# Performance work log

Measured on AMD Instinct MI355X. Metric: run time of the kernel, lower is better.

Reference implementation:

```python
import jax, jax.numpy as jnp
import numpy as np

N = 100000
E = 3200000
CH_IN = 128
HID = 128
CH_OUT = 3


def setup_inputs() -> dict:
    key = jax.random.key(0)
    ks = jax.random.split(key, 16)
    def lin(kw, fan_in, fan_out):
        bound = 1.0 / np.sqrt(fan_in)
        kw1, kw2 = jax.random.split(kw)
        W = jax.random.uniform(kw1, (fan_in, fan_out), jnp.float32, -bound, bound)
        b = jax.random.uniform(kw2, (fan_out,), jnp.float32, -bound, bound)
        return W, b
    x = jax.random.normal(ks[0], (N, CH_IN), jnp.float32)
    edge_index = jax.random.randint(ks[1], (2, E), 0, N, jnp.int64)
    W1, b1 = lin(ks[2], CH_IN, HID)
    W2, b2 = lin(ks[3], HID, HID)
    lw1, lb1 = lin(ks[4], HID, HID)
    lw2, lb2 = lin(ks[5], HID, HID)
    lw3, lb3 = lin(ks[6], HID, HID)
    lw4, lb4 = lin(ks[7], HID, CH_OUT)
    return {"x": x, "edge_index": edge_index,
            "W1": W1, "b1": b1, "W2": W2, "b2": b2,
            "lw1": lw1, "lb1": lb1, "lw2": lw2, "lb2": lb2,
            "lw3": lw3, "lb3": lb3, "lw4": lw4, "lb4": lb4}


def gcn_conv(x, W, b, src, dst, n_nodes):
    xw = x @ W  # [N, H]
    ew = jnp.ones(src.shape[0], x.dtype)
    deg = jax.ops.segment_sum(ew, dst, num_segments=n_nodes) + 2.0  # +2 from improved self-loop
    dinv = jnp.where(deg > 0, jax.lax.rsqrt(deg), 0.0)
    norm = dinv[src] * dinv[dst]  # [E]
    agg = jax.ops.segment_sum(xw[src] * norm[:, None], dst, num_segments=n_nodes)
    # self-loop contribution: weight 2 * dinv[i]^2 * xw[i]
    agg = agg + xw * (2.0 * dinv * dinv)[:, None]
    return agg + b


def reference(x, edge_index, W1, b1, W2, b2, lw1, lb1, lw2, lb2, lw3, lb3, lw4, lb4):
    src, dst = edge_index[0], edge_index[1]
    n = x.shape[0]
    h = jnp.tanh(gcn_conv(x, W1, b1, src, dst, n))
    h = jnp.tanh(gcn_conv(h, W2, b2, src, dst, n))
    # dropout in eval mode = identity
    h = jnp.tanh(h @ lw1 + lb1)
    h = jnp.tanh(h @ lw2 + lb2)
    h = jnp.tanh(h @ lw3 + lb3)
    return h @ lw4 + lb4
```

## Files before the change

### kernel.cpp

```cpp
#include <hip/hip_runtime.h>

typedef __attribute__((ext_vector_type(8))) short short8;
typedef __attribute__((ext_vector_type(4))) float floatx4;
typedef __attribute__((ext_vector_type(4))) unsigned int uintx4;
typedef unsigned int uint32;

__device__ inline float b2f(unsigned short u) {
    union { uint32 i; float f; } x; x.i = ((uint32)u) << 16; return x.f;
}
__device__ inline float bl(uint32 v) {
    union { uint32 i; float f; } x; x.i = v << 16; return x.f;
}
__device__ inline float bh(uint32 v) {
    union { uint32 i; float f; } x; x.i = v & 0xffff0000u; return x.f;
}
__device__ inline unsigned short f2b(float f) {
    union { float f; uint32 u; } x; x.f = f;
    uint32 r = x.u + 0x7fffu + ((x.u >> 16) & 1u);
    return (unsigned short)(r >> 16);
}
__device__ inline float fast_tanh(float x) {
    float ax = __builtin_fabsf(x);
    float t = __builtin_amdgcn_exp2f(-2.8853900817779268f * ax);
    float r = (1.0f - t) * __builtin_amdgcn_rcpf(1.0f + t);
    return __builtin_copysignf(r, x);
}


#define CHUNK 8192
#define MAXBK 512
#define CAP   8704

__global__ __launch_bounds__(512, 2) void scatterb_k(const int* __restrict__ eidx,
                                                     uint32* __restrict__ bkt_cur,
                                                     uint32* __restrict__ packed, int E) {
    __shared__ uint32 hist[MAXBK];
    __shared__ uint32 ssum[MAXBK];
    __shared__ uint32 hsc[MAXBK];
    __shared__ uint32 gbase[MAXBK];
    __shared__ uint32 lcur[MAXBK];
    __shared__ uint32 stage[CHUNK];
    __shared__ unsigned short stgb[CHUNK];
    int t = threadIdx.x;
    int cbase = blockIdx.x * CHUNK;
    int n = E - cbase; if (n > CHUNK) n = CHUNK;

    hist[t] = 0;
    __syncthreads();
    int dreg[CHUNK / 512];
    int nt = 0;
    for (int i = t; i < n; i += 512) {
        int d = eidx[E + cbase + i];
        dreg[nt++] = d;
        atomicAdd(&hist[d >> 8], 1u);
    }
    __syncthreads();
    uint32 v = hist[t];
    ssum[t] = v;
    __syncthreads();
    for (int off = 1; off < MAXBK; off <<= 1) {
        uint32 x = (t >= off) ? ssum[t - off] : 0;
        __syncthreads();
        ssum[t] += x;
        __syncthreads();
    }
    uint32 excl = ssum[t] - v;
    hsc[t] = excl;
    lcur[t] = excl;
    if (v) gbase[t] = atomicAdd(&bkt_cur[t], v);
    __syncthreads();
    nt = 0;
    for (int i = t; i < n; i += 512) {
        int s = eidx[cbase + i];
        int d = dreg[nt++];
        int b = d >> 8;
        uint32 pos = atomicAdd(&lcur[b], 1u);
        stage[pos] = ((uint32)s << 8) | (uint32)(d & 255);
        stgb[pos] = (unsigned short)b;
    }
    __syncthreads();
    for (int i = t; i < n; i += 512) {
        int b = stgb[i];
        packed[gbase[b] + (i - hsc[b])] = stage[i];
    }
}

__global__ __launch_bounds__(256) void buildb_k(const uint32* __restrict__ packed,
                                                const uint32* __restrict__ bkt_cur,
                                                int* __restrict__ rowp,
                                                int* __restrict__ rowe,
                                                float* __restrict__ dinv,
                                                int* __restrict__ csr, int N) {
    __shared__ uint32 cnt[256];
    __shared__ uint32 incl[256];
    __shared__ uint32 cur[256];
    int t = threadIdx.x;
    int b = blockIdx.x;
    uint32 base = (uint32)b * CAP;
    uint32 size = bkt_cur[b] - base;
    int node0 = b << 8;

    cnt[t] = 0;
    __syncthreads();
    for (uint32 i = t; i < size; i += 256)
        atomicAdd(&cnt[packed[base + i] & 255u], 1u);
    __syncthreads();
    uint32 v = cnt[t];
    incl[t] = v;
    __syncthreads();
    for (int off = 1; off < 256; off <<= 1) {
        uint32 x = (t >= off) ? incl[t - off] : 0;
        __syncthreads();
        incl[t] += x;
        __syncthreads();
    }
    uint32 loc = incl[t] - v;
    cur[t] = loc;
    int node = node0 + t;
    if (node < N) {
        dinv[node] = rsqrtf((float)v + 2.0f);
        rowp[node] = (int)(base + loc);
        rowe[node] = (int)(base + loc + v);
    }
    __syncthreads();
    for (uint32 i = t; i < size; i += 256) {
        uint32 p = packed[base + i];
        uint32 pos = atomicAdd(&cur[p & 255u], 1u);
        csr[base + pos] = (int)(p >> 8);
    }
}


__global__ __launch_bounds__(256) void prep_w5_k(const float* __restrict__ w0,
                                                 const float* __restrict__ w1,
                                                 const float* __restrict__ w2,
                                                 const float* __restrict__ w3,
                                                 const float* __restrict__ w4,
                                                 unsigned short* __restrict__ Wt_hi,
                                                 unsigned short* __restrict__ Wt_lo,
                                                 uint32* __restrict__ bkt_cur) {
    if (blockIdx.x < 2) {
        int idx = blockIdx.x * 256 + threadIdx.x;
        bkt_cur[idx] = (uint32)idx * CAP;
    }
    int t = blockIdx.x * 256 + threadIdx.x;
    int widx = t >> 11;
    int f8 = t & 2047;
    const float* W;
    switch (widx) {
        case 0: W = w0; break;
        case 1: W = w1; break;
        case 2: W = w2; break;
        case 3: W = w3; break;
        default: W = w4; break;
    }
    int ct = f8 >> 8, kc = (f8 >> 6) & 3, quad = (f8 >> 4) & 3, r = f8 & 15;
    int c = ct * 16 + r;
    int kbase = kc * 32 + quad * 8;
    short8 hi8, lo8;
#pragma unroll
    for (int j = 0; j < 8; ++j) {
        float w = W[(kbase + j) * 128 + c];
        unsigned short h = f2b(w);
        hi8[j] = (short)h;
        lo8[j] = (short)f2b(w - b2f(h));
    }
    *(short8*)(Wt_hi + widx * 16384 + f8 * 8) = hi8;
    *(short8*)(Wt_lo + widx * 16384 + f8 * 8) = lo8;
}


template <int ASRC>
__global__ __launch_bounds__(256, 4) void gemm_z_k(
    const void* __restrict__ Asrc,
    const unsigned short* __restrict__ Wt_hi,
    const unsigned short* __restrict__ Wt_lo,
    const float* __restrict__ dinv,
    unsigned short* __restrict__ out, int N) {
    int tid = threadIdx.x;
    int wave = tid >> 6, lane = tid & 63;
    int quad = lane >> 4, r = lane & 15;
    int m32 = blockIdx.x * 128 + wave * 32;

    short8 af[2][4];
#pragma unroll
    for (int s = 0; s < 2; ++s) {
        int rowA = m32 + s * 16 + r;
        if (rowA >= N) rowA = N - 1;
        if (ASRC == 0) {
            const float4* Af = (const float4*)Asrc;
#pragma unroll
            for (int kc = 0; kc < 4; ++kc) {
                float4 p0 = Af[((size_t)rowA * 128 + kc * 32 + quad * 8) >> 2];
                float4 p1 = Af[(((size_t)rowA * 128 + kc * 32 + quad * 8) >> 2) + 1];
                short8 a;
                a[0] = (short)f2b(p0.x); a[1] = (short)f2b(p0.y);
                a[2] = (short)f2b(p0.z); a[3] = (short)f2b(p0.w);
                a[4] = (short)f2b(p1.x); a[5] = (short)f2b(p1.y);
                a[6] = (short)f2b(p1.z); a[7] = (short)f2b(p1.w);
                af[s][kc] = a;
            }
        } else {
            const short* Ap = (const short*)Asrc;
#pragma unroll
            for (int kc = 0; kc < 4; ++kc)
                af[s][kc] = *(const short8*)(Ap + (size_t)rowA * 128 + kc * 32 + quad * 8);
        }
    }

    float dv[2][4];
#pragma unroll
    for (int s = 0; s < 2; ++s)
#pragma unroll
        for (int reg = 0; reg < 4; ++reg) {
            int i = m32 + s * 16 + quad * 4 + reg;
            dv[s][reg] = dinv[i < N ? i : N - 1];
        }

    const short8* WhF = (const short8*)Wt_hi + lane;
    const short8* WlF = (const short8*)Wt_lo + lane;

#pragma unroll
    for (int ct = 0; ct < 8; ++ct) {
        int n = ct * 16 + r;
        floatx4 a0 = {0.f, 0.f, 0.f, 0.f}, a1 = {0.f, 0.f, 0.f, 0.f};
#pragma unroll
        for (int kc = 0; kc < 4; ++kc) {
            short8 bh8 = WhF[(ct * 4 + kc) << 6];
            a0 = __builtin_amdgcn_mfma_f32_16x16x32_bf16(af[0][kc], bh8, a0, 0, 0, 0);
            a1 = __builtin_amdgcn_mfma_f32_16x16x32_bf16(af[1][kc], bh8, a1, 0, 0, 0);
            short8 bl8 = WlF[(ct * 4 + kc) << 6];
            a0 = __builtin_amdgcn_mfma_f32_16x16x32_bf16(af[0][kc], bl8, a0, 0, 0, 0);
            a1 = __builtin_amdgcn_mfma_f32_16x16x32_bf16(af[1][kc], bl8, a1, 0, 0, 0);
        }
#pragma unroll
        for (int reg = 0; reg < 4; ++reg) {
            int i0 = m32 + quad * 4 + reg;
            if (i0 < N) out[(size_t)i0 * 128 + n] = f2b(a0[reg] * dv[0][reg]);
            int i1 = m32 + 16 + quad * 4 + reg;
            if (i1 < N) out[(size_t)i1 * 128 + n] = f2b(a1[reg] * dv[1][reg]);
        }
    }
}


#define LSTR 136

__global__ __launch_bounds__(256, 2) void mlp_fused_k(
    const unsigned short* __restrict__ H,
    const unsigned short* __restrict__ WH,
    const unsigned short* __restrict__ WL,
    const float* __restrict__ lb1, const float* __restrict__ lb2,
    const float* __restrict__ lb3,
    const float* __restrict__ W4, const float* __restrict__ b4,
    float* __restrict__ out, int N) {
    __shared__ __align__(16) unsigned short wbuf[16384];
    __shared__ __align__(16) unsigned short tile[4][32 * LSTR];
    __shared__ float w4s[384];
    int tid = threadIdx.x;
    if (tid < 192) { w4s[tid] = W4[tid]; w4s[tid + 192] = W4[tid + 192]; }

    int wave = tid >> 6, lane = tid & 63;
    int quad = lane >> 4, r = lane & 15;
    unsigned short* T = tile[wave];
    int m32 = blockIdx.x * 128 + wave * 32;

    short8 af[2][4];
    const short* Hp = (const short*)H;
#pragma unroll
    for (int s = 0; s < 2; ++s) {
        int rowA = m32 + s * 16 + r;
        if (rowA >= N) rowA = N - 1;
#pragma unroll
        for (int kc = 0; kc < 4; ++kc)
            af[s][kc] = *(const short8*)(Hp + (size_t)rowA * 128 + kc * 32 + quad * 8);
    }

    const float* biases[3] = {lb1, lb2, lb3};
#pragma unroll
    for (int L = 0; L < 3; ++L) {
        const float* bias = biases[L];
        float bvv[8];
#pragma unroll
        for (int ct = 0; ct < 8; ++ct) bvv[ct] = bias[ct * 16 + r];
#pragma unroll
        for (int hf = 0; hf < 2; ++hf) {
            __syncthreads();
            {
                const uintx4* sh = (const uintx4*)(WH + L * 16384 + hf * 8192);
                const uintx4* sl = (const uintx4*)(WL + L * 16384 + hf * 8192);
                uintx4* dh = (uintx4*)wbuf;
                uintx4* dl = (uintx4*)(wbuf + 8192);
#pragma unroll
                for (int it = 0; it < 4; ++it) dh[tid + it * 256] = sh[tid + it * 256];
#pragma unroll
                for (int it = 0; it < 4; ++it) dl[tid + it * 256] = sl[tid + it * 256];
            }
            __syncthreads();
            const short8* whF = (const short8*)wbuf + lane;
            const short8* wlF = (const short8*)(wbuf + 8192) + lane;
#pragma unroll
            for (int c2 = 0; c2 < 4; ++c2) {
                int ct = hf * 4 + c2;
                int n = ct * 16 + r;
                floatx4 a0 = {0.f, 0.f, 0.f, 0.f}, a1 = {0.f, 0.f, 0.f, 0.f};
#pragma unroll
                for (int kc = 0; kc < 4; ++kc) {
                    short8 bh8 = whF[(c2 * 4 + kc) << 6];
                    a0 = __builtin_amdgcn_mfma_f32_16x16x32_bf16(af[0][kc], bh8, a0, 0, 0, 0);
                    a1 = __builtin_amdgcn_mfma_f32_16x16x32_bf16(af[1][kc], bh8, a1, 0, 0, 0);
                    short8 bl8 = wlF[(c2 * 4 + kc) << 6];
                    a0 = __builtin_amdgcn_mfma_f32_16x16x32_bf16(af[0][kc], bl8, a0, 0, 0, 0);
                    a1 = __builtin_amdgcn_mfma_f32_16x16x32_bf16(af[1][kc], bl8, a1, 0, 0, 0);
                }
                float bv = bvv[ct];
#pragma unroll
                for (int reg = 0; reg < 4; ++reg) {
                    int lrow = quad * 4 + reg;
                    T[lrow * LSTR + n] = f2b(fast_tanh(a0[reg] + bv));
                    T[(lrow + 16) * LSTR + n] = f2b(fast_tanh(a1[reg] + bv));
                }
            }
        }
        if (L < 2) {
#pragma unroll
            for (int s = 0; s < 2; ++s)
#pragma unroll
                for (int kc = 0; kc < 4; ++kc)
                    af[s][kc] = *(const short8*)&T[(s * 16 + r) * LSTR + kc * 32 + quad * 8];
        }
    }

    int lrow = lane & 31;
    int halfc = lane >> 5;
    float a0 = 0.f, a1 = 0.f, a2 = 0.f;
#pragma unroll
    for (int c8 = 0; c8 < 8; ++c8) {
        int cbase = halfc * 64 + c8 * 8;
        short8 hv = *(const short8*)&T[lrow * LSTR + cbase];
#pragma unroll
        for (int j = 0; j < 8; ++j) {
            float xv = b2f((unsigned short)hv[j]);
            int ch = cbase + j;
            a0 = fmaf(xv, w4s[ch * 3 + 0], a0);
            a1 = fmaf(xv, w4s[ch * 3 + 1], a1);
            a2 = fmaf(xv, w4s[ch * 3 + 2], a2);
        }
    }
    a0 += __shfl_xor(a0, 32);
    a1 += __shfl_xor(a1, 32);
    a2 += __shfl_xor(a2, 32);
    if (halfc == 0) {
        int i = m32 + lrow;
        if (i < N) {
            out[(size_t)i * 3 + 0] = a0 + b4[0];
            out[(size_t)i * 3 + 1] = a1 + b4[1];
            out[(size_t)i * 3 + 2] = a2 + b4[2];
        }
    }
}


__global__ __launch_bounds__(256) void agg_full_k(
    const uint32* __restrict__ z, const int* __restrict__ rowp,
    const int* __restrict__ rowe, const int* __restrict__ csr,
    const float* __restrict__ dinv, const float* __restrict__ bias,
    uint32* __restrict__ out, int N) {
    int lane = threadIdx.x & 63;
    int i = blockIdx.x * 4 + (threadIdx.x >> 6);
    if (i >= N) return;
    int start = rowp[i], end = rowe[i];
    const uint32* zl = z + lane;
    float a0 = 0.f, a1 = 0.f;
    for (int e = start; e < end; e += 64) {
        int cnt = end - e;
        if (cnt > 64) cnt = 64;
        int s = (lane < cnt) ? csr[e + lane] : N;
        int mp = (cnt + 15) & ~15;
        for (int m = 0; m < mp; m += 16) {
            uint32 v[16];
#pragma unroll
            for (int p = 0; p < 16; ++p) {
                int sj = __shfl(s, m + p);
                v[p] = zl[(size_t)sj << 6];
            }
#pragma unroll
            for (int p = 0; p < 16; ++p) {
                a0 += bl(v[p]);
                a1 += bh(v[p]);
            }
        }
    }
    uint32 vi = zl[(size_t)i << 6];
    a0 += 2.f * bl(vi);
    a1 += 2.f * bh(vi);
    float di = dinv[i];
    float2 bv = ((const float2*)bias)[lane];
    float h0 = fast_tanh(fmaf(di, a0, bv.x));
    float h1 = fast_tanh(fmaf(di, a1, bv.y));
    out[((size_t)i << 6) + lane] = (uint32)f2b(h0) | ((uint32)f2b(h1) << 16);
}

extern "C" void kernel_launch(void* const* d_in, const int* in_sizes, int n_in,
                              void* d_out, int out_size, void* d_ws, size_t ws_size,
                              hipStream_t stream) {
    const float* x   = (const float*)d_in[0];
    const int* eidx  = (const int*)d_in[1];
    const float* W1  = (const float*)d_in[2];
    const float* b1  = (const float*)d_in[3];
    const float* W2  = (const float*)d_in[4];
    const float* b2  = (const float*)d_in[5];
    const float* lw1 = (const float*)d_in[6];
    const float* lb1 = (const float*)d_in[7];
    const float* lw2 = (const float*)d_in[8];
    const float* lb2 = (const float*)d_in[9];
    const float* lw3 = (const float*)d_in[10];
    const float* lb3 = (const float*)d_in[11];
    const float* lw4 = (const float*)d_in[12];
    const float* lb4 = (const float*)d_in[13];
    float* out = (float*)d_out;

    const int N = in_sizes[0] / 128;
    const int E = in_sizes[1] / 2;

    char* p = (char*)d_ws;
    auto alloc = [&](size_t bytes) -> void* {
        void* q = (void*)p;
        p += (bytes + 255) & ~(size_t)255;
        return q;
    };
    const int NBK = (N + 255) >> 8;
    float* dinv      = (float*)alloc((size_t)N * 4);
    int* rowp        = (int*)alloc((size_t)N * 4);
    int* rowe        = (int*)alloc((size_t)N * 4);
    uint32* bkt_cur  = (uint32*)alloc(MAXBK * 4);
    int* csr         = (int*)alloc((size_t)NBK * CAP * 4);
    unsigned short* Wt_hi = (unsigned short*)alloc(5 * 16384 * 2);
    unsigned short* Wt_lo = (unsigned short*)alloc(5 * 16384 * 2);
    unsigned short* bufA  = (unsigned short*)alloc((size_t)(N + 1) * 128 * 2);
    unsigned short* bufB  = (unsigned short*)alloc((size_t)(N + 1) * 128 * 2);
    uint32* packed = (uint32*)bufA;

    const int MB4 = (N + 127) / 128;
    const int AB  = (N + 3) / 4;
    const int NCH = (E + CHUNK - 1) / CHUNK;

    hipMemsetAsync(bufA + (size_t)N * 128, 0, 256, stream);
    prep_w5_k<<<40, 256, 0, stream>>>(W1, W2, lw1, lw2, lw3, Wt_hi, Wt_lo, bkt_cur);
    scatterb_k<<<NCH, 512, 0, stream>>>(eidx, bkt_cur, packed, E);
    buildb_k<<<NBK, 256, 0, stream>>>(packed, bkt_cur, rowp, rowe, dinv, csr, N);

    const unsigned short* WH = Wt_hi;
    const unsigned short* WL = Wt_lo;

    gemm_z_k<0><<<MB4, 256, 0, stream>>>(x, WH + 0 * 16384, WL + 0 * 16384, dinv, bufA, N);
    agg_full_k<<<AB, 256, 0, stream>>>((const uint32*)bufA, rowp, rowe, csr, dinv, b1,
                                       (uint32*)bufB, N);
    gemm_z_k<1><<<MB4, 256, 0, stream>>>(bufB, WH + 1 * 16384, WL + 1 * 16384, dinv, bufA, N);
    agg_full_k<<<AB, 256, 0, stream>>>((const uint32*)bufA, rowp, rowe, csr, dinv, b2,
                                       (uint32*)bufB, N);
    mlp_fused_k<<<MB4, 256, 0, stream>>>(bufB, WH + 2 * 16384, WL + 2 * 16384,
                                         lb1, lb2, lb3, lw4, lb4, out, N);
}
```

Measured before the change: 453.8 us.

## Split SpMM aggregation into eight feature-slice passes for cache locality

Replaces the single full-row aggregation kernel with eight launches, each gathering only a 16-channel (32-byte) slice of every neighbour row. A wave handles eight neighbours at once in groups of eight lanes and reduces across lanes with shuffles. The aim is to keep each pass's working set (N×32 bytes) resident in L2/MALL, so the random gathers hit cache instead of DRAM. In exchange it adds launches, re-reads the CSR structure eight times, issues narrower 32-byte gathers, and leaves most lanes idle during the epilogue. The v[8] array is indexed dynamically and may spill to scratch.

```diff
diff --git a/kernel.cpp b/kernel.cpp
--- a/kernel.cpp
+++ b/kernel.cpp
@@ -361,44 +361,47 @@
 }
 
 
-__global__ __launch_bounds__(256) void agg_full_k(
+__global__ __launch_bounds__(256) void agg_slice_k(
     const uint32* __restrict__ z, const int* __restrict__ rowp,
     const int* __restrict__ rowe, const int* __restrict__ csr,
     const float* __restrict__ dinv, const float* __restrict__ bias,
-    uint32* __restrict__ out, int N) {
+    uint32* __restrict__ out, int N, int pass) {
     int lane = threadIdx.x & 63;
+    int g = lane >> 3, c = lane & 7;
     int i = blockIdx.x * 4 + (threadIdx.x >> 6);
     if (i >= N) return;
     int start = rowp[i], end = rowe[i];
-    const uint32* zl = z + lane;
+    const uint32* zs = z + pass * 8 + c;
     float a0 = 0.f, a1 = 0.f;
     for (int e = start; e < end; e += 64) {
         int cnt = end - e;
         if (cnt > 64) cnt = 64;
         int s = (lane < cnt) ? csr[e + lane] : N;
-        int mp = (cnt + 15) & ~15;
-        for (int m = 0; m < mp; m += 16) {
-            uint32 v[16];
-#pragma unroll
-            for (int p = 0; p < 16; ++p) {
-                int sj = __shfl(s, m + p);
-                v[p] = zl[(size_t)sj << 6];
-            }
-#pragma unroll
-            for (int p = 0; p < 16; ++p) {
-                a0 += bl(v[p]);
-                a1 += bh(v[p]);
-            }
-        }
-    }
-    uint32 vi = zl[(size_t)i << 6];
-    a0 += 2.f * bl(vi);
-    a1 += 2.f * bh(vi);
-    float di = dinv[i];
-    float2 bv = ((const float2*)bias)[lane];
-    float h0 = fast_tanh(fmaf(di, a0, bv.x));
-    float h1 = fast_tanh(fmaf(di, a1, bv.y));
-    out[((size_t)i << 6) + lane] = (uint32)f2b(h0) | ((uint32)f2b(h1) << 16);
+        int nb = (cnt + 7) >> 3;
+        uint32 v[8];
+        for (int b = 0; b < nb; ++b) {
+            int sj = __shfl(s, b * 8 + g);
+            v[b] = zs[(size_t)sj << 6];
+        }
+        for (int b = 0; b < nb; ++b) {
+            a0 += bl(v[b]);
+            a1 += bh(v[b]);
+        }
+    }
+    a0 += __shfl_xor(a0, 8);  a1 += __shfl_xor(a1, 8);
+    a0 += __shfl_xor(a0, 16); a1 += __shfl_xor(a1, 16);
+    a0 += __shfl_xor(a0, 32); a1 += __shfl_xor(a1, 32);
+    if (lane < 8) {
+        uint32 vi = zs[(size_t)i << 6];
+        a0 += 2.f * bl(vi);
+        a1 += 2.f * bh(vi);
+        float di = dinv[i];
+        float2 bv = ((const float2*)bias)[pass * 8 + lane];
+        float h0 = fast_tanh(fmaf(di, a0, bv.x));
+        float h1 = fast_tanh(fmaf(di, a1, bv.y));
+        out[((size_t)i << 6) + pass * 8 + lane] =
+            (uint32)f2b(h0) | ((uint32)f2b(h1) << 16);
+    }
 }
 
 extern "C" void kernel_launch(void* const* d_in, const int* in_sizes, int n_in,
@@ -454,11 +457,13 @@
     const unsigned short* WL = Wt_lo;
 
     gemm_z_k<0><<<MB4, 256, 0, stream>>>(x, WH + 0 * 16384, WL + 0 * 16384, dinv, bufA, N);
-    agg_full_k<<<AB, 256, 0, stream>>>((const uint32*)bufA, rowp, rowe, csr, dinv, b1,
-                                       (uint32*)bufB, N);
+    for (int pass = 0; pass < 8; ++pass)
+        agg_slice_k<<<AB, 256, 0, stream>>>((const uint32*)bufA, rowp, rowe, csr,
+                                            dinv, b1, (uint32*)bufB, N, pass);
     gemm_z_k<1><<<MB4, 256, 0, stream>>>(bufB, WH + 1 * 16384, WL + 1 * 16384, dinv, bufA, N);
-    agg_full_k<<<AB, 256, 0, stream>>>((const uint32*)bufA, rowp, rowe, csr, dinv, b2,
-                                       (uint32*)bufB, N);
+    for (int pass = 0; pass < 8; ++pass)
+        agg_slice_k<<<AB, 256, 0, stream>>>((const uint32*)bufA, rowp, rowe, csr,
+                                            dinv, b2, (uint32*)bufB, N, pass);
     mlp_fused_k<<<MB4, 256, 0, stream>>>(bufB, WH + 2 * 16384, WL + 2 * 16384,
                                          lb1, lb2, lb3, lw4, lb4, out, N);
 }
```

Measured after the change: 1.194 ms. 2.63x slower.
